# Kernel optimization log

Hardware: AMD Instinct MI355X
Metric: run time of the kernel (lower is better)

The kernel has to match this reference:

```python
import jax, jax.numpy as jnp
from jax import lax
import numpy as np


def setup_inputs() -> dict:
    key = jax.random.key(0)
    kx, kw = jax.random.split(key)
    # Binary {0,1} activations: the module's int8-cast/XOR/AND trick is only
    # meaningful XNOR-popcount math for binary inputs.
    x = jax.random.randint(kx, (32, 256, 58, 58), 0, 2).astype(jnp.float32)
    weight = jax.random.normal(kw, (256, 256, 3, 3), dtype=jnp.float32)
    return {"x": x, "weight": weight}


def reference(x, weight):
    # XNORConv2d.forward, stride=1, padding=0 (forward never pads).
    B, C, H, W = x.shape
    O, _, kh, kw = weight.shape
    n = C * H * W  # note: alpha normalizes by INPUT size, as in the source
    N = kh * kw

    # alpha = sum_{c,kh,kw} |w| / n, one scalar per output filter  -> (O,)
    alpha = jnp.sum(jnp.abs(weight), axis=(1, 2, 3)) / n

    # Binarized weights: sign(w) >= 0 -> {0,1}
    bw = (weight >= 0).astype(x.dtype)

    dn = lax.conv_dimension_numbers(x.shape, weight.shape, ("NCHW", "OIHW", "NCHW"))
    conv = lambda a, f: lax.conv_general_dilated(
        a, f, window_strides=(1, 1), padding="VALID", dimension_numbers=dn
    )

    # XNOR match count per (b, o, y, x): S = #(p==f) over c,kh,kw
    #   = conv(p, f) + conv(1-p, 1-f)
    S = conv(x, bw) + conv(1.0 - x, 1.0 - bw)  # (B, O, H', W')

    # popcount per channel = 2*s_c - N; summed over channels -> 2*S - C*N
    res = 2.0 * S - jnp.asarray(C * N, dtype=x.dtype)

    return alpha[None, :, None, None] * res
```

## Files before the change

kernel.cpp:

```cpp
#include <hip/hip_runtime.h>
#include <stdint.h>


#define BATCH 32
#define C_IN 256
#define OCH 256
#define HIN 58
#define WIN2 58
#define HOUT 56
#define WOUT 56
#define TAPS 9
#define WWORDS 8
#define HWIN (HIN * WIN2)
#define HWOUT (HOUT * WOUT)
#define NPOS (BATCH * HWIN)

typedef unsigned int u32x8 __attribute__((ext_vector_type(8)));

#define XA0(xs, wv) { uint32_t _t;                                        \
    asm("v_xor_b32 %0, %2, %3\n\tv_bcnt_u32_b32 %1, %0, %1"               \
        : "=&v"(_t), "+v"(a0) : "s"(xs), "v"(wv)); }
#define XA1(xs, wv) { uint32_t _t;                                        \
    asm("v_xor_b32 %0, %2, %3\n\tv_bcnt_u32_b32 %1, %0, %1"               \
        : "=&v"(_t), "+v"(a1) : "s"(xs), "v"(wv)); }

__global__ __launch_bounds__(256) void pack_x_kernel(
    const float* __restrict__ x, uint32_t* __restrict__ xp)
{
    int t = blockIdx.x * 256 + threadIdx.x;
    int p  = t >> 2;
    int wp = t & 3;
    int b = p / HWIN;
    int r = p - b * HWIN;
    const float* xb = x + ((size_t)(b * C_IN + wp * 64)) * HWIN + r;
    uint32_t m0 = 0u, m1 = 0u;
    #pragma unroll
    for (int j = 0; j < 32; ++j) {
        float v0 = xb[(size_t)j * HWIN];
        float v1 = xb[(size_t)(j + 32) * HWIN];
        m0 |= (v0 > 0.5f ? 1u : 0u) << j;
        m1 |= (v1 > 0.5f ? 1u : 0u) << j;
    }
    *(uint2*)(xp + (size_t)p * WWORDS + wp * 2) = make_uint2(m0, m1);
}

__global__ __launch_bounds__(256) void pack_w_kernel(
    const float* __restrict__ wt, uint32_t* __restrict__ wq,
    float* __restrict__ sA, float* __restrict__ sB)
{
    int o = blockIdx.x;
    int c = threadIdx.x;
    const float* wb = wt + ((size_t)o * C_IN + c) * TAPS;
    float wv[TAPS];
    float s = 0.f;
    #pragma unroll
    for (int t = 0; t < TAPS; ++t) {
        wv[t] = wb[t];
        s += fabsf(wv[t]);
    }
    int wave = c >> 6, lane = c & 63;
    #pragma unroll
    for (int t = 0; t < TAPS; ++t) {
        unsigned long long m = __ballot(wv[t] >= 0.0f);
        if (lane == 0) {
            wq[(size_t)(t * 8 + wave * 2)     * OCH + o] = (uint32_t)m;
            wq[(size_t)(t * 8 + wave * 2 + 1) * OCH + o] = (uint32_t)(m >> 32);
        }
    }
    __shared__ float red[256];
    red[c] = s;
    __syncthreads();
    for (int off = 128; off > 0; off >>= 1) {
        if (c < off) red[c] += red[c + off];
        __syncthreads();
    }
    if (c == 0) {
        float alpha = red[0] / (float)(C_IN * HWIN);
        sA[o] = -2.0f * alpha;
        sB[o] = (float)(C_IN * TAPS) * alpha;
    }
}

__global__ __launch_bounds__(256)
__attribute__((amdgpu_waves_per_eu(4, 4)))
void xnor_main_kernel(
    const uint32_t* __restrict__ xp, const uint32_t* __restrict__ wq,
    const float* __restrict__ sA, const float* __restrict__ sB,
    float* __restrict__ out)
{
    __shared__ float olds[64 * 57];

    int rj = blockIdx.x;
    int b  = rj / HOUT;
    int oy = rj - b * HOUT;
    int obase = blockIdx.y * 64;
    int lane = threadIdx.x & 63;
    int wv_id = __builtin_amdgcn_readfirstlane((int)(threadIdx.x >> 6));
    int o = obase + lane;

    uint32_t wreg[72];
    #pragma unroll
    for (int i = 0; i < 72; ++i)
        wreg[i] = wq[(size_t)i * OCH + o];
    float sAv = sA[o];
    float sBv = sB[o];

    int ox0 = wv_id * 14;

    const uint32_t* r0 = xp + (((size_t)b * HIN + oy + 0) * WIN2 + ox0) * WWORDS;
    const uint32_t* r1 = xp + (((size_t)b * HIN + oy + 1) * WIN2 + ox0) * WWORDS;
    const uint32_t* r2 = xp + (((size_t)b * HIN + oy + 2) * WIN2 + ox0) * WWORDS;

    u32x8 W0a = *(const u32x8*)(r0);
    u32x8 W0b = *(const u32x8*)(r0 + 8);
    u32x8 W0c = *(const u32x8*)(r0 + 16);
    u32x8 W1a = *(const u32x8*)(r1);
    u32x8 W1b = *(const u32x8*)(r1 + 8);
    u32x8 W1c = *(const u32x8*)(r1 + 16);
    u32x8 W2a = *(const u32x8*)(r2);
    u32x8 W2b = *(const u32x8*)(r2 + 8);
    u32x8 W2c = *(const u32x8*)(r2 + 16);

    #pragma unroll 1
    for (int i = 0; i < 14; ++i) {
        uint32_t a0 = 0u, a1 = 0u;
        #pragma unroll
        for (int k = 0; k < 8; ++k) XA0(W0a[k], wreg[0 * 8 + k]);
        #pragma unroll
        for (int k = 0; k < 8; ++k) XA1(W0b[k], wreg[1 * 8 + k]);
        #pragma unroll
        for (int k = 0; k < 8; ++k) XA0(W0c[k], wreg[2 * 8 + k]);
        r0 += 8;
        W0a = *(const u32x8*)(r0);
        W0b = *(const u32x8*)(r0 + 8);
        W0c = *(const u32x8*)(r0 + 16);
        #pragma unroll
        for (int k = 0; k < 8; ++k) XA1(W1a[k], wreg[3 * 8 + k]);
        #pragma unroll
        for (int k = 0; k < 8; ++k) XA0(W1b[k], wreg[4 * 8 + k]);
        #pragma unroll
        for (int k = 0; k < 8; ++k) XA1(W1c[k], wreg[5 * 8 + k]);
        r1 += 8;
        W1a = *(const u32x8*)(r1);
        W1b = *(const u32x8*)(r1 + 8);
        W1c = *(const u32x8*)(r1 + 16);
        #pragma unroll
        for (int k = 0; k < 8; ++k) XA0(W2a[k], wreg[6 * 8 + k]);
        #pragma unroll
        for (int k = 0; k < 8; ++k) XA1(W2b[k], wreg[7 * 8 + k]);
        #pragma unroll
        for (int k = 0; k < 8; ++k) XA0(W2c[k], wreg[8 * 8 + k]);
        r2 += 8;
        W2a = *(const u32x8*)(r2);
        W2b = *(const u32x8*)(r2 + 8);
        W2c = *(const u32x8*)(r2 + 16);

        float P = (float)(a0 + a1);
        olds[lane * 57 + (ox0 + i)] = fmaf(sAv, P, sBv);
    }

    __syncthreads();

    size_t obb = ((size_t)b * OCH + obase) * HWOUT + (size_t)oy * WOUT;
    int tau = threadIdx.x;
    #pragma unroll 1
    for (int i = 0; i < 14; ++i) {
        int flat = i * 256 + tau;
        int op = flat / 56;
        int pp = flat - op * 56;
        out[obb + (size_t)op * HWOUT + pp] = olds[op * 57 + pp];
    }
}

extern "C" void kernel_launch(void* const* d_in, const int* in_sizes, int n_in,
                              void* d_out, int out_size, void* d_ws, size_t ws_size,
                              hipStream_t stream)
{
    const float* x  = (const float*)d_in[0];
    const float* wt = (const float*)d_in[1];
    float* out = (float*)d_out;

    char* ws = (char*)d_ws;
    uint32_t* xp = (uint32_t*)ws;
    uint32_t* wq = (uint32_t*)(ws + 3444736);
    float*    sA = (float*)(ws + 3444736 + 73728);
    float*    sB = (float*)(ws + 3444736 + 73728 + 1024);

    pack_x_kernel<<<dim3(1682), dim3(256), 0, stream>>>(x, xp);

    pack_w_kernel<<<dim3(OCH), dim3(256), 0, stream>>>(wt, wq, sA, sB);

    xnor_main_kernel<<<dim3(1792, 4), dim3(256), 0, stream>>>(xp, wq, sA, sB, out);
}
```

Baseline: 296.0 us.

## Restructure main loop row-major with sliding window and per-row weight registers

The main kernel now processes one input row at a time. It loads only 24 weight words per row instead of holding all 72 in registers, and keeps 14 accumulator pairs live across the three rows. Within each row a sliding window reuses the previous two input columns, so each packed pixel is loaded once instead of three times. The loops are fully unrolled. This aims to cut VGPR pressure and redundant scalar loads, at the cost of reloading weights per row and a much larger code footprint.

```diff
diff --git a/kernel.cpp b/kernel.cpp
--- a/kernel.cpp
+++ b/kernel.cpp
@@ -17,12 +17,9 @@
 
 typedef unsigned int u32x8 __attribute__((ext_vector_type(8)));
 
-#define XA0(xs, wv) { uint32_t _t;                                        \
+#define XA(accv, xs, wv) { uint32_t _t;                                   \
     asm("v_xor_b32 %0, %2, %3\n\tv_bcnt_u32_b32 %1, %0, %1"               \
-        : "=&v"(_t), "+v"(a0) : "s"(xs), "v"(wv)); }
-#define XA1(xs, wv) { uint32_t _t;                                        \
-    asm("v_xor_b32 %0, %2, %3\n\tv_bcnt_u32_b32 %1, %0, %1"               \
-        : "=&v"(_t), "+v"(a1) : "s"(xs), "v"(wv)); }
+        : "=&v"(_t), "+v"(accv) : "s"(xs), "v"(wv)); }
 
 __global__ __launch_bounds__(256) void pack_x_kernel(
     const float* __restrict__ x, uint32_t* __restrict__ xp)
@@ -98,64 +95,49 @@
     int wv_id = __builtin_amdgcn_readfirstlane((int)(threadIdx.x >> 6));
     int o = obase + lane;
 
-    uint32_t wreg[72];
-    #pragma unroll
-    for (int i = 0; i < 72; ++i)
-        wreg[i] = wq[(size_t)i * OCH + o];
     float sAv = sA[o];
     float sBv = sB[o];
 
     int ox0 = wv_id * 14;
 
-    const uint32_t* r0 = xp + (((size_t)b * HIN + oy + 0) * WIN2 + ox0) * WWORDS;
-    const uint32_t* r1 = xp + (((size_t)b * HIN + oy + 1) * WIN2 + ox0) * WWORDS;
-    const uint32_t* r2 = xp + (((size_t)b * HIN + oy + 2) * WIN2 + ox0) * WWORDS;
+    uint32_t accA[14], accB[14];
+    #pragma unroll
+    for (int i = 0; i < 14; ++i) { accA[i] = 0u; accB[i] = 0u; }
 
-    u32x8 W0a = *(const u32x8*)(r0);
-    u32x8 W0b = *(const u32x8*)(r0 + 8);
-    u32x8 W0c = *(const u32x8*)(r0 + 16);
-    u32x8 W1a = *(const u32x8*)(r1);
-    u32x8 W1b = *(const u32x8*)(r1 + 8);
-    u32x8 W1c = *(const u32x8*)(r1 + 16);
-    u32x8 W2a = *(const u32x8*)(r2);
-    u32x8 W2b = *(const u32x8*)(r2 + 8);
-    u32x8 W2c = *(const u32x8*)(r2 + 16);
+#define DO_ROW(r)                                                         \
+    {                                                                     \
+        uint32_t wrow[24];                                                \
+        _Pragma("unroll")                                                 \
+        for (int k = 0; k < 24; ++k)                                      \
+            wrow[k] = wq[(size_t)((r) * 24 + k) * OCH + o];               \
+        const uint32_t* rp = xp +                                         \
+            (((size_t)b * HIN + oy + (r)) * WIN2 + ox0) * WWORDS;         \
+        u32x8 c0 = *(const u32x8*)(rp);                                   \
+        u32x8 c1 = *(const u32x8*)(rp + 8);                               \
+        _Pragma("unroll")                                                 \
+        for (int i = 0; i < 14; ++i) {                                    \
+            u32x8 c2 = *(const u32x8*)(rp + (size_t)(i + 2) * 8);         \
+            _Pragma("unroll")                                             \
+            for (int k = 0; k < 8; ++k)                                   \
+                XA(((k & 1) ? accB[i] : accA[i]), c0[k], wrow[k]);        \
+            _Pragma("unroll")                                             \
+            for (int k = 0; k < 8; ++k)                                   \
+                XA(((k & 1) ? accB[i] : accA[i]), c1[k], wrow[8 + k]);    \
+            _Pragma("unroll")                                             \
+            for (int k = 0; k < 8; ++k)                                   \
+                XA(((k & 1) ? accB[i] : accA[i]), c2[k], wrow[16 + k]);   \
+            c0 = c1; c1 = c2;                                             \
+        }                                                                 \
+    }
 
-    #pragma unroll 1
+    DO_ROW(0)
+    DO_ROW(1)
+    DO_ROW(2)
+#undef DO_ROW
+
+    #pragma unroll
     for (int i = 0; i < 14; ++i) {
-        uint32_t a0 = 0u, a1 = 0u;
-        #pragma unroll
-        for (int k = 0; k < 8; ++k) XA0(W0a[k], wreg[0 * 8 + k]);
-        #pragma unroll
-        for (int k = 0; k < 8; ++k) XA1(W0b[k], wreg[1 * 8 + k]);
-        #pragma unroll
-        for (int k = 0; k < 8; ++k) XA0(W0c[k], wreg[2 * 8 + k]);
-        r0 += 8;
-        W0a = *(const u32x8*)(r0);
-        W0b = *(const u32x8*)(r0 + 8);
-        W0c = *(const u32x8*)(r0 + 16);
-        #pragma unroll
-        for (int k = 0; k < 8; ++k) XA1(W1a[k], wreg[3 * 8 + k]);
-        #pragma unroll
-        for (int k = 0; k < 8; ++k) XA0(W1b[k], wreg[4 * 8 + k]);
-        #pragma unroll
-        for (int k = 0; k < 8; ++k) XA1(W1c[k], wreg[5 * 8 + k]);
-        r1 += 8;
-        W1a = *(const u32x8*)(r1);
-        W1b = *(const u32x8*)(r1 + 8);
-        W1c = *(const u32x8*)(r1 + 16);
-        #pragma unroll
-        for (int k = 0; k < 8; ++k) XA0(W2a[k], wreg[6 * 8 + k]);
-        #pragma unroll
-        for (int k = 0; k < 8; ++k) XA1(W2b[k], wreg[7 * 8 + k]);
-        #pragma unroll
-        for (int k = 0; k < 8; ++k) XA0(W2c[k], wreg[8 * 8 + k]);
-        r2 += 8;
-        W2a = *(const u32x8*)(r2);
-        W2b = *(const u32x8*)(r2 + 8);
-        W2c = *(const u32x8*)(r2 + 16);
-
-        float P = (float)(a0 + a1);
+        float P = (float)(accA[i] + accB[i]);
         olds[lane * 57 + (ox0 + i)] = fmaf(sAv, P, sBv);
     }
 
```

Measured after the change: 303.5 us. +2.5%, slower.
